# Kernel optimization log

Measured on AMD Instinct MI355X. Metric: run time of the kernel, lower is better.

The kernel has to match this reference:

```python
import jax, jax.numpy as jnp
import numpy as np


def setup_inputs() -> dict:
    key = jax.random.key(0)
    k1, k2 = jax.random.split(key)
    B, T, D = 32, 512, 512
    x = jax.random.normal(k1, (B, T, D), dtype=jnp.float32)
    duration = jax.random.randint(k2, (B, T), 0, 8, dtype=jnp.int64)
    return {"x": x, "duration": duration, "max_len": 4096}


def reference(x, duration, max_len):
    # x: [B, T, D]; duration: [B, T] ints; output: [B, max_len, D]
    B, T, D = x.shape
    csum = jnp.cumsum(duration, axis=1)            # [B, T] end offsets per phoneme
    mel_len = csum[:, -1].astype(jnp.int64)        # [B]
    frames = jnp.arange(max_len)                   # [L]
    # frame j belongs to phoneme i where csum[i-1] <= j < csum[i]
    # == searchsorted(csum, j, side='right')
    idx = jax.vmap(lambda c: jnp.searchsorted(c, frames, side='right'))(csum)  # [B, L]
    idx_c = jnp.minimum(idx, T - 1)                # clamp out-of-range (padded region)
    out = jnp.take_along_axis(x, idx_c[..., None], axis=1)  # [B, L, D]
    mask = frames[None, :] < mel_len[:, None]      # [B, L] valid frames
    out = out * mask[..., None].astype(x.dtype)    # zero-pad beyond mel_len
    return out, mel_len
```

## Files before the change

### kernel.cpp

```cpp
#include <hip/hip_runtime.h>
#include <hip/hip_bf16.h>


typedef float f32x4 __attribute__((ext_vector_type(4)));

constexpr int B   = 32;
constexpr int T   = 512;
constexpr int D   = 512;
constexpr int D4  = D / 4;
constexpr int ML  = 4096;
constexpr int CHUNK    = 128;
constexpr int NTHREADS = 512;

__global__ __launch_bounds__(NTHREADS) void lr_fused(
    const int*   __restrict__ duration,
    const f32x4* __restrict__ x,
    f32x4*       __restrict__ out,
    float*       __restrict__ mel_out)
{
    constexpr int NCHUNK = ML / CHUNK;
    const int b     = blockIdx.x / NCHUNK;
    const int chunk = blockIdx.x % NCHUNK;
    const int j0    = chunk * CHUNK;
    const int t     = threadIdx.x;
    const int lane  = t & 63;
    const int wave  = t >> 6;

    __shared__ int csum[T];
    __shared__ int wsum[NTHREADS / 64];
    __shared__ int sidx[CHUNK];

    int v = duration[b * T + t];
    #pragma unroll
    for (int off = 1; off < 64; off <<= 1) {
        int n = __shfl_up(v, off, 64);
        if (lane >= off) v += n;
    }
    if (t < CHUNK) sidx[t] = -1;
    if (lane == 63) wsum[wave] = v;
    __syncthreads();

    int prev = 0;
    #pragma unroll
    for (int w = 0; w < NTHREADS / 64; ++w)
        if (w < wave) prev += wsum[w];
    v += prev;
    csum[t] = v;
    __syncthreads();

    const int end   = v;
    const int start = (t == 0) ? 0 : csum[t - 1];
    const int mel   = csum[T - 1];

    const int lo = start > j0 ? start : j0;
    const int hi = end < j0 + CHUNK ? end : j0 + CHUNK;
    for (int j = lo; j < hi; ++j)
        sidx[j - j0] = t;
    __syncthreads();

    if (chunk == 0 && t == 0)
        mel_out[b] = (float)mel;

    const size_t obase = (size_t)(b * ML + j0) * D4;
    const size_t xbase = (size_t)b * T * D4;
    const f32x4 zero = {0.f, 0.f, 0.f, 0.f};

    #pragma unroll 8
    for (int i = 0; i < (CHUNK * D4) / NTHREADS; ++i) {
        const int m   = i * NTHREADS + t;
        const int f   = m >> 7;
        const int d4  = m & (D4 - 1);
        const int row = sidx[f];
        f32x4 val = (row >= 0) ? x[xbase + (size_t)row * D4 + d4] : zero;
        __builtin_nontemporal_store(val, &out[obase + m]);
    }
}

extern "C" void kernel_launch(void* const* d_in, const int* in_sizes, int n_in,
                              void* d_out, int out_size, void* d_ws, size_t ws_size,
                              hipStream_t stream) {
    const float* x   = (const float*)d_in[0];
    const int*   dur = (const int*)d_in[1];

    float* out     = (float*)d_out;
    float* mel_out = out + (size_t)B * ML * D;

    lr_fused<<<B * (ML / CHUNK), NTHREADS, 0, stream>>>(
        dur, (const f32x4*)x, (f32x4*)out, mel_out);
}
```

Measured before the change: 58.53 us.

## Split work into phoneme-centric expand blocks and separate zero-pad blocks

Replaces the frame-chunk gather with phoneme-centric blocks. Each wave loads one phoneme row of x into registers once and writes it to every output frame it covers. Separate blocks zero-fill the padded region past mel_len and exit early when a chunk is fully valid. This cuts redundant x reads and the shared-memory index table. In exchange, per-wave work is uneven because durations vary, and stores are no longer nontemporal.

```diff
diff --git a/kernel.cpp b/kernel.cpp
--- a/kernel.cpp
+++ b/kernel.cpp
@@ -9,26 +9,27 @@
 constexpr int D   = 512;
 constexpr int D4  = D / 4;
 constexpr int ML  = 4096;
-constexpr int CHUNK    = 128;
 constexpr int NTHREADS = 512;
+constexpr int kPhonPerBlock = 8;
+constexpr int kNumExp  = T / kPhonPerBlock;
+constexpr int kZChunk  = 512;
+constexpr int kNumZero = ML / kZChunk;
+constexpr int kBlocksPerBatch = kNumExp + kNumZero;
 
-__global__ __launch_bounds__(NTHREADS) void lr_fused(
+__global__ __launch_bounds__(NTHREADS) void lr_expand(
     const int*   __restrict__ duration,
     const f32x4* __restrict__ x,
     f32x4*       __restrict__ out,
     float*       __restrict__ mel_out)
 {
-    constexpr int NCHUNK = ML / CHUNK;
-    const int b     = blockIdx.x / NCHUNK;
-    const int chunk = blockIdx.x % NCHUNK;
-    const int j0    = chunk * CHUNK;
-    const int t     = threadIdx.x;
-    const int lane  = t & 63;
-    const int wave  = t >> 6;
+    const int b    = blockIdx.x / kBlocksPerBatch;
+    const int r    = blockIdx.x % kBlocksPerBatch;
+    const int t    = threadIdx.x;
+    const int lane = t & 63;
+    const int wave = t >> 6;
 
     __shared__ int csum[T];
     __shared__ int wsum[NTHREADS / 64];
-    __shared__ int sidx[CHUNK];
 
     int v = duration[b * T + t];
     #pragma unroll
@@ -36,10 +37,8 @@
         int n = __shfl_up(v, off, 64);
         if (lane >= off) v += n;
     }
-    if (t < CHUNK) sidx[t] = -1;
     if (lane == 63) wsum[wave] = v;
     __syncthreads();
-
     int prev = 0;
     #pragma unroll
     for (int w = 0; w < NTHREADS / 64; ++w)
@@ -48,31 +47,37 @@
     csum[t] = v;
     __syncthreads();
 
-    const int end   = v;
-    const int start = (t == 0) ? 0 : csum[t - 1];
-    const int mel   = csum[T - 1];
+    const int mel = csum[T - 1];
 
-    const int lo = start > j0 ? start : j0;
-    const int hi = end < j0 + CHUNK ? end : j0 + CHUNK;
-    for (int j = lo; j < hi; ++j)
-        sidx[j - j0] = t;
-    __syncthreads();
+    if (r < kNumExp) {
+        const int p     = r * kPhonPerBlock + wave;
+        const int end   = csum[p];
+        const int start = (p == 0) ? 0 : csum[p - 1];
 
-    if (chunk == 0 && t == 0)
-        mel_out[b] = (float)mel;
+        if (r == 0 && t == 0)
+            mel_out[b] = (float)mel;
 
-    const size_t obase = (size_t)(b * ML + j0) * D4;
-    const size_t xbase = (size_t)b * T * D4;
-    const f32x4 zero = {0.f, 0.f, 0.f, 0.f};
-
-    #pragma unroll 8
-    for (int i = 0; i < (CHUNK * D4) / NTHREADS; ++i) {
-        const int m   = i * NTHREADS + t;
-        const int f   = m >> 7;
-        const int d4  = m & (D4 - 1);
-        const int row = sidx[f];
-        f32x4 val = (row >= 0) ? x[xbase + (size_t)row * D4 + d4] : zero;
-        __builtin_nontemporal_store(val, &out[obase + m]);
+        if (end > start) {
+            const size_t xoff = ((size_t)(b * T + p)) * D4 + 2 * lane;
+            const f32x4 v0 = x[xoff];
+            const f32x4 v1 = x[xoff + 1];
+            size_t o = ((size_t)(b * ML + start)) * D4 + 2 * lane;
+            for (int j = start; j < end; ++j, o += D4) {
+                out[o]     = v0;
+                out[o + 1] = v1;
+            }
+        }
+    } else {
+        const int c  = r - kNumExp;
+        const int j0 = c * kZChunk;
+        int fstart = mel - j0;
+        if (fstart >= kZChunk) return;
+        if (fstart < 0) fstart = 0;
+        const int total = (kZChunk - fstart) * D4;
+        const size_t base = ((size_t)(b * ML + j0 + fstart)) * D4;
+        const f32x4 zero = {0.f, 0.f, 0.f, 0.f};
+        for (int m = t; m < total; m += NTHREADS)
+            out[base + m] = zero;
     }
 }
 
@@ -85,6 +90,6 @@
     float* out     = (float*)d_out;
     float* mel_out = out + (size_t)B * ML * D;
 
-    lr_fused<<<B * (ML / CHUNK), NTHREADS, 0, stream>>>(
+    lr_expand<<<B * kBlocksPerBatch, NTHREADS, 0, stream>>>(
         dur, (const f32x4*)x, (f32x4*)out, mel_out);
 }
```

Result: slower. 64.14 us (+9.6%).
